# Optimization experiments

Hardware: AMD Instinct MI355X
Metric: run time of the kernel (lower is better)

The kernel has to match this reference:

```python
import jax, jax.numpy as jnp
import numpy as np

DIM, K_NN, RADIUS, HIDDEN = 128, 4, 2.5, 64
B, T, N = 32, 64, 25


def setup_inputs() -> dict:
    key = jax.random.key(0)
    ks = jax.random.split(key, 12)
    s = 0.02
    return {
        "emb": jax.random.normal(ks[0], (B, T, N, DIM), jnp.float32),
        "bboxes": jax.random.uniform(ks[1], (B, T, N, 4), jnp.float32),
        "person_mask": jax.random.uniform(ks[2], (B, T, N)) < 0.9,
        "edge_w1": jax.random.normal(ks[3], (2 * DIM + 3, HIDDEN), jnp.float32) * s,
        "edge_b1": jnp.zeros((HIDDEN,), jnp.float32),
        "edge_w2": jax.random.normal(ks[4], (HIDDEN, DIM), jnp.float32) * s,
        "edge_b2": jnp.zeros((DIM,), jnp.float32),
        "node_w1": jax.random.normal(ks[5], (2 * DIM, HIDDEN), jnp.float32) * s,
        "node_b1": jnp.zeros((HIDDEN,), jnp.float32),
        "node_w2": jax.random.normal(ks[6], (HIDDEN, DIM), jnp.float32) * s,
        "node_b2": jnp.zeros((DIM,), jnp.float32),
        "ln_g": jnp.ones((DIM,), jnp.float32),
        "ln_b": jnp.zeros((DIM,), jnp.float32),
    }


def _forward(emb, bboxes, person_mask, edge_w1, edge_b1, edge_w2, edge_b2,
             node_w1, node_b1, node_w2, node_b2, ln_g, ln_b):
    b, t, n, d = emb.shape
    BT = b * t
    x = emb.reshape(BT, n, d)
    boxes = bboxes.reshape(BT, n, 4)
    mask = person_mask.reshape(BT, n)

    cx, cy = boxes[..., 0], boxes[..., 1]
    h = jnp.maximum(boxes[..., 3], 1e-6)
    dx = cx[:, :, None] - cx[:, None, :]            # [BT,N,N]
    dy = cy[:, :, None] - cy[:, None, :]
    dist = jnp.sqrt(dx * dx + dy * dy + 1e-6)
    scale = h[:, :, None]
    dx_n, dy_n, dist_n = dx / scale, dy / scale, dist / scale

    eye = jnp.eye(n, dtype=bool)[None]
    pair_valid = (mask[:, :, None] & mask[:, None, :]) & ~eye
    dist_for_knn = jnp.where(pair_valid, dist_n, 1e6)

    K = min(K_NN, max(n - 1, 1))
    neg_d, knn_idx = jax.lax.top_k(-dist_for_knn, K)  # smallest-K -> [BT,N,K]
    knn_dist = -neg_d

    nbr_valid = jnp.take_along_axis(pair_valid, knn_idx, axis=2)
    nbr_valid = nbr_valid & (knn_dist < RADIUS)

    # gather neighbor features: [BT,N,K,D]
    bt_idx = jnp.arange(BT)[:, None, None]
    x_j = x[bt_idx, knn_idx]
    x_i = jnp.broadcast_to(x[:, :, None, :], (BT, n, K, d))
    edge_all = jnp.stack([dx_n, dy_n, dist_n], axis=-1)  # [BT,N,N,3]
    e_ij = jnp.take_along_axis(edge_all, knn_idx[..., None], axis=2)  # [BT,N,K,3]

    msg_in = jnp.concatenate([x_i, x_j, e_ij], axis=-1)  # [BT,N,K,2D+3]
    msg = jax.nn.relu(msg_in @ edge_w1 + edge_b1) @ edge_w2 + edge_b2
    nbr_f = nbr_valid.astype(msg.dtype)
    msg = msg * nbr_f[..., None]
    denom = jnp.maximum(nbr_f.sum(axis=2, keepdims=True), 1.0)
    agg = msg.sum(axis=2) / denom                    # [BT,N,D]

    upd_in = jnp.concatenate([x, agg], axis=-1)
    delta = jax.nn.relu(upd_in @ node_w1 + node_b1) @ node_w2 + node_b2
    has_nbr = jnp.any(nbr_valid, axis=2, keepdims=True)
    delta = delta * has_nbr.astype(delta.dtype)

    y = x + delta
    mu = y.mean(axis=-1, keepdims=True)
    var = y.var(axis=-1, keepdims=True)
    y = (y - mu) * jax.lax.rsqrt(var + 1e-5) * ln_g + ln_b
    out = y * mask[..., None].astype(y.dtype)
    return out.reshape(b, t, n, d)


def reference(emb, bboxes, person_mask, edge_w1, edge_b1, edge_w2, edge_b2,
              node_w1, node_b1, node_w2, node_b2, ln_g, ln_b):
    return _forward(emb, bboxes, person_mask, edge_w1, edge_b1, edge_w2, edge_b2,
                    node_w1, node_b1, node_w2, node_b2, ln_g, ln_b)
```

## Files before the change

kernel.cpp:

```cpp
#include <hip/hip_runtime.h>

#define NN   25
#define DD   128
#define HH   64
#define KK   4
#define RADF 2.5f

#define XBP  136
#define HSP  72
#define AGP  136

#define O_W1T 0
#define O_W2T 16896
#define O_N1T 25088
#define O_N2T 41472

typedef __attribute__((ext_vector_type(8))) short  short8;
typedef __attribute__((ext_vector_type(4))) float  f32x4;

__device__ __forceinline__ ushort f2bf(float x) {
    uint u = __float_as_uint(x);
    u += 0x7fffu + ((u >> 16) & 1u);
    return (ushort)(u >> 16);
}
__device__ __forceinline__ float bf2f(ushort u) {
    return __uint_as_float((uint)u << 16);
}
__device__ __forceinline__ uint pack2(float a, float b) {
    return (uint)f2bf(a) | ((uint)f2bf(b) << 16);
}
__device__ __forceinline__ short8 ldw(const ushort* p) {
    return *reinterpret_cast<const short8*>(p);
}
#define MFMA16(a, b, c) __builtin_amdgcn_mfma_f32_16x16x32_bf16((a), (b), (c), 0, 0, 0)

__global__ void prep_kernel(const float* __restrict__ ew1, const float* __restrict__ ew2,
                            const float* __restrict__ nw1, const float* __restrict__ nw2,
                            ushort* __restrict__ w) {
    int tid = blockIdx.x * blockDim.x + threadIdx.x;
    int stride = gridDim.x * blockDim.x;
    for (int e = tid; e < 259 * 64; e += stride) {
        int k = e >> 6, c = e & 63;
        w[O_W1T + c * 264 + k] = f2bf(ew1[e]);
    }
    for (int e = tid; e < 64 * 128; e += stride) {
        int k = e >> 7, d = e & 127;
        w[O_W2T + d * 64 + k] = f2bf(ew2[e]);
    }
    for (int e = tid; e < 256 * 64; e += stride) {
        int k = e >> 6, c = e & 63;
        w[O_N1T + c * 256 + k] = f2bf(nw1[e]);
    }
    for (int e = tid; e < 64 * 128; e += stride) {
        int k = e >> 7, d = e & 127;
        w[O_N2T + d * 64 + k] = f2bf(nw2[e]);
    }
}

__global__ __launch_bounds__(64, 2) void ig9_kernel(
    const float* __restrict__ emb,
    const float* __restrict__ bboxes,
    const int*   __restrict__ pmask,
    const float* __restrict__ ew1f,
    const float* __restrict__ eb1,
    const float* __restrict__ eb2,
    const float* __restrict__ nb1,
    const float* __restrict__ nb2,
    const float* __restrict__ lng,
    const float* __restrict__ lnb,
    const ushort* __restrict__ W,
    float* __restrict__ out)
{
    const int bt  = blockIdx.x;
    const int ln  = threadIdx.x;
    const int g   = ln >> 4;
    const int r16 = ln & 15;

    __shared__ ushort s_xb[NN * XBP];
    __shared__ __align__(16) char s_R[7200];
    __shared__ ushort s_g1v[NN * HSP];
    __shared__ float  s_ev[NN][KK][4];
    __shared__ short  s_idxs[NN][KK];
    __shared__ float  s_meta[NN][4];

    ushort* s_hxi = reinterpret_cast<ushort*>(s_R);
    ushort* s_hs  = reinterpret_cast<ushort*>(s_R + 3600);
    ushort* s_ag  = reinterpret_cast<ushort*>(s_R);

    {
        const float4* src4 = reinterpret_cast<const float4*>(emb + (size_t)bt * (NN * DD));
        for (int u = ln; u < NN * 16; u += 64) {
            int row = u >> 4, q = u & 15;
            float4 f0 = src4[row * 32 + q * 2];
            float4 f1 = src4[row * 32 + q * 2 + 1];
            uint4 p;
            p.x = pack2(f0.x, f0.y); p.y = pack2(f0.z, f0.w);
            p.z = pack2(f1.x, f1.y); p.w = pack2(f1.z, f1.w);
            *reinterpret_cast<uint4*>(&s_xb[row * XBP + q * 8]) = p;
        }
    }

    {
        const int n = (ln < NN) ? ln : NN - 1;
        const float4 b4 = *reinterpret_cast<const float4*>(bboxes + ((size_t)bt * NN + n) * 4);
        const float cxn = b4.x, cyn = b4.y;
        const float hvn = fmaxf(b4.w, 1e-6f);
        const int   mn  = pmask[(size_t)bt * NN + n];
        const float inv = 1.0f / hvn;
        float best[KK] = {1e30f, 1e30f, 1e30f, 1e30f};
        int   bidx[KK] = {0, 0, 0, 0};
        for (int j = 0; j < NN; ++j) {
            float cxj = __shfl(cxn, j);
            float cyj = __shfl(cyn, j);
            int   mj  = __shfl(mn, j);
            float dx = cxn - cxj, dy = cyn - cyj;
            float dn = sqrtf(fmaf(dx, dx, fmaf(dy, dy, 1e-6f))) * inv;
            bool  pv = (mn != 0) && (mj != 0) && (j != n);
            float cv = pv ? dn : 1e6f;
            int   ci = j;
#pragma unroll
            for (int kk = 0; kk < KK; ++kk) {
                if (cv < best[kk]) {
                    float tv = best[kk]; best[kk] = cv; cv = tv;
                    int   ti = bidx[kk]; bidx[kk] = ci; ci = ti;
                }
            }
        }
        float cnt = 0.f;
        float e0v[KK], e1v[KK], e2v[KK], vvv[KK];
#pragma unroll
        for (int k = 0; k < KK; ++k) {
            int bj = bidx[k];
            float cxb = __shfl(cxn, bj);
            float cyb = __shfl(cyn, bj);
            float val = (best[k] < RADF) ? 1.f : 0.f;
            cnt += val;
            float dx = cxn - cxb, dy = cyn - cyb;
            e0v[k] = dx * inv;
            e1v[k] = dy * inv;
            e2v[k] = sqrtf(fmaf(dx, dx, fmaf(dy, dy, 1e-6f))) * inv;
            vvv[k] = val;
        }
        if (ln < NN) {
#pragma unroll
            for (int k = 0; k < KK; ++k) {
                s_ev[n][k][0] = e0v[k];
                s_ev[n][k][1] = e1v[k];
                s_ev[n][k][2] = e2v[k];
                s_ev[n][k][3] = vvv[k];
                s_idxs[n][k]  = (short)bidx[k];
            }
            s_meta[n][0] = cnt;
            s_meta[n][1] = 1.0f / fmaxf(cnt, 1.0f);
            s_meta[n][2] = (cnt > 0.f) ? 1.f : 0.f;
            s_meta[n][3] = mn ? 1.f : 0.f;
        }
    }
    __syncthreads();

    {
        int na1 = 16 + r16; if (na1 > 24) na1 = 24;
        const ushort* A0 = s_xb + r16 * XBP + g * 8;
        const ushort* A1 = s_xb + na1 * XBP + g * 8;
        f32x4 c[2][4] = {};
#pragma unroll
        for (int kt = 0; kt < 4; ++kt) {
            short8 b[4];
#pragma unroll
            for (int nt = 0; nt < 4; ++nt)
                b[nt] = ldw(W + O_W1T + (size_t)(16 * nt + r16) * 264 + kt * 32 + g * 8);
            short8 a0 = ldw(A0 + kt * 32);
            short8 a1 = ldw(A1 + kt * 32);
#pragma unroll
            for (int nt = 0; nt < 4; ++nt) {
                c[0][nt] = MFMA16(a0, b[nt], c[0][nt]);
                c[1][nt] = MFMA16(a1, b[nt], c[1][nt]);
            }
        }
#pragma unroll
        for (int mt = 0; mt < 2; ++mt)
#pragma unroll
            for (int q = 0; q < 4; ++q) {
                int nr = 16 * mt + 4 * g + q;
                if (nr < 25) {
#pragma unroll
                    for (int nt = 0; nt < 4; ++nt)
                        s_hxi[nr * HSP + 16 * nt + r16] = f2bf(c[mt][nt][q]);
                }
            }
    }
    __syncthreads();

    {
        int jn[7];
#pragma unroll
        for (int T = 0; T < 7; ++T) {
            int r = 16 * T + r16; if (r > 99) r = 99;
            jn[T] = s_idxs[r >> 2][r & 3];
        }
        f32x4 c[7][4] = {};
#pragma unroll
        for (int kt = 0; kt < 4; ++kt) {
            short8 b[4];
#pragma unroll
            for (int nt = 0; nt < 4; ++nt)
                b[nt] = ldw(W + O_W1T + (size_t)(16 * nt + r16) * 264 + 128 + kt * 32 + g * 8);
#pragma unroll
            for (int T = 0; T < 7; ++T) {
                short8 a = ldw(s_xb + jn[T] * XBP + kt * 32 + g * 8);
#pragma unroll
                for (int nt = 0; nt < 4; ++nt)
                    c[T][nt] = MFMA16(a, b[nt], c[T][nt]);
            }
        }
        float we0[4], we1[4], we2[4], bb1[4];
#pragma unroll
        for (int nt = 0; nt < 4; ++nt) {
            int col = 16 * nt + r16;
            we0[nt] = ew1f[256 * 64 + col];
            we1[nt] = ew1f[257 * 64 + col];
            we2[nt] = ew1f[258 * 64 + col];
            bb1[nt] = eb1[col];
        }
#pragma unroll
        for (int T = 0; T < 7; ++T) {
            const int n = 4 * T + g;
            if (n < 25) {
                float v0 = s_ev[n][0][3], v1 = s_ev[n][1][3];
                float v2 = s_ev[n][2][3], v3 = s_ev[n][3][3];
                float e0q[4], e1q[4], e2q[4];
#pragma unroll
                for (int q = 0; q < 4; ++q) {
                    e0q[q] = s_ev[n][q][0]; e1q[q] = s_ev[n][q][1]; e2q[q] = s_ev[n][q][2];
                }
#pragma unroll
                for (int nt = 0; nt < 4; ++nt) {
                    int col = 16 * nt + r16;
                    float base = bb1[nt] + bf2f(s_hxi[n * HSP + col]);
                    float p0 = c[T][nt][0] + base + e0q[0] * we0[nt] + e1q[0] * we1[nt] + e2q[0] * we2[nt];
                    float p1 = c[T][nt][1] + base + e0q[1] * we0[nt] + e1q[1] * we1[nt] + e2q[1] * we2[nt];
                    float p2 = c[T][nt][2] + base + e0q[2] * we0[nt] + e1q[2] * we1[nt] + e2q[2] * we2[nt];
                    float p3 = c[T][nt][3] + base + e0q[3] * we0[nt] + e1q[3] * we1[nt] + e2q[3] * we2[nt];
                    float hs = fmaf(v0, fmaxf(p0, 0.f),
                               fmaf(v1, fmaxf(p1, 0.f),
                               fmaf(v2, fmaxf(p2, 0.f),
                                    v3 * fmaxf(p3, 0.f))));
                    s_hs[n * HSP + col] = f2bf(hs);
                }
            }
        }
    }
    __syncthreads();

    {
        int na1 = 16 + r16; if (na1 > 24) na1 = 24;
        const ushort* A0 = s_hs + r16 * HSP + g * 8;
        const ushort* A1 = s_hs + na1 * HSP + g * 8;
        f32x4 c[2][8] = {};
#pragma unroll
        for (int kt = 0; kt < 2; ++kt) {
            short8 a0 = ldw(A0 + kt * 32);
            short8 a1 = ldw(A1 + kt * 32);
#pragma unroll
            for (int nt = 0; nt < 8; ++nt) {
                short8 b = ldw(W + O_W2T + (size_t)(16 * nt + r16) * 64 + kt * 32 + g * 8);
                c[0][nt] = MFMA16(a0, b, c[0][nt]);
                c[1][nt] = MFMA16(a1, b, c[1][nt]);
            }
        }
        __syncthreads();
#pragma unroll
        for (int nt = 0; nt < 8; ++nt) {
            int col = 16 * nt + r16;
            float b2c = eb2[col];
#pragma unroll
            for (int mt = 0; mt < 2; ++mt)
#pragma unroll
                for (int q = 0; q < 4; ++q) {
                    int nr = 16 * mt + 4 * g + q;
                    if (nr < 25) {
                        float agv = s_meta[nr][1] * fmaf(s_meta[nr][0], b2c, c[mt][nt][q]);
                        s_ag[nr * AGP + col] = f2bf(agv);
                    }
                }
        }
    }
    __syncthreads();

    {
        int na1 = 16 + r16; if (na1 > 24) na1 = 24;
        const ushort* Ax0 = s_xb + r16 * XBP + g * 8;
        const ushort* Ax1 = s_xb + na1 * XBP + g * 8;
        const ushort* Aa0 = s_ag + r16 * AGP + g * 8;
        const ushort* Aa1 = s_ag + na1 * AGP + g * 8;
        f32x4 c[2][4] = {};
#pragma unroll
        for (int kt = 0; kt < 8; ++kt) {
            const ushort* Ap0 = (kt < 4) ? (Ax0 + kt * 32) : (Aa0 + (kt - 4) * 32);
            const ushort* Ap1 = (kt < 4) ? (Ax1 + kt * 32) : (Aa1 + (kt - 4) * 32);
            short8 a0 = ldw(Ap0);
            short8 a1 = ldw(Ap1);
#pragma unroll
            for (int nt = 0; nt < 4; ++nt) {
                short8 b = ldw(W + O_N1T + (size_t)(16 * nt + r16) * 256 + kt * 32 + g * 8);
                c[0][nt] = MFMA16(a0, b, c[0][nt]);
                c[1][nt] = MFMA16(a1, b, c[1][nt]);
            }
        }
#pragma unroll
        for (int nt = 0; nt < 4; ++nt) {
            int col = 16 * nt + r16;
            float b1c = nb1[col];
#pragma unroll
            for (int mt = 0; mt < 2; ++mt)
#pragma unroll
                for (int q = 0; q < 4; ++q) {
                    int nr = 16 * mt + 4 * g + q;
                    if (nr < 25)
                        s_g1v[nr * HSP + col] = f2bf(fmaxf(c[mt][nt][q] + b1c, 0.f));
                }
        }
    }
    __syncthreads();

    {
        int na1 = 16 + r16; if (na1 > 24) na1 = 24;
        const ushort* A0 = s_g1v + r16 * HSP + g * 8;
        const ushort* A1 = s_g1v + na1 * HSP + g * 8;
        f32x4 c[2][8] = {};
#pragma unroll
        for (int kt = 0; kt < 2; ++kt) {
            short8 a0 = ldw(A0 + kt * 32);
            short8 a1 = ldw(A1 + kt * 32);
#pragma unroll
            for (int nt = 0; nt < 8; ++nt) {
                short8 b = ldw(W + O_N2T + (size_t)(16 * nt + r16) * 64 + kt * 32 + g * 8);
                c[0][nt] = MFMA16(a0, b, c[0][nt]);
                c[1][nt] = MFMA16(a1, b, c[1][nt]);
            }
        }
        float nb2c[8], glc[8], blc[8];
#pragma unroll
        for (int nt = 0; nt < 8; ++nt) {
            int col = 16 * nt + r16;
            nb2c[nt] = nb2[col];
            glc[nt]  = lng[col];
            blc[nt]  = lnb[col];
        }
#pragma unroll
        for (int mt = 0; mt < 2; ++mt) {
#pragma unroll
            for (int q = 0; q < 4; ++q) {
                int nr = 16 * mt + 4 * g + q;
                int nc = nr < 25 ? nr : 24;
                float has = s_meta[nc][2];
                float y[8];
                float a = 0.f, b = 0.f;
#pragma unroll
                for (int nt = 0; nt < 8; ++nt) {
                    int col = 16 * nt + r16;
                    float yv = fmaf(has, c[mt][nt][q] + nb2c[nt], bf2f(s_xb[nc * XBP + col]));
                    y[nt] = yv;
                    a += yv;
                    b = fmaf(yv, yv, b);
                }
#pragma unroll
                for (int o = 1; o < 16; o <<= 1) {
                    a += __shfl_xor(a, o);
                    b += __shfl_xor(b, o);
                }
                float mu  = a * (1.0f / 128.0f);
                float var = b * (1.0f / 128.0f) - mu * mu;
                float rs  = rsqrtf(var + 1e-5f);
                float mk  = s_meta[nc][3];
                if (nr < 25) {
                    float* op = out + (size_t)bt * (NN * DD) + nr * DD;
#pragma unroll
                    for (int nt = 0; nt < 8; ++nt) {
                        int col = 16 * nt + r16;
                        op[col] = fmaf((y[nt] - mu) * rs, glc[nt], blc[nt]) * mk;
                    }
                }
            }
        }
    }
}

extern "C" void kernel_launch(void* const* d_in, const int* in_sizes, int n_in,
                              void* d_out, int out_size, void* d_ws, size_t ws_size,
                              hipStream_t stream) {
    const float* emb    = (const float*)d_in[0];
    const float* bboxes = (const float*)d_in[1];
    const int*   pmask  = (const int*)  d_in[2];
    const float* ew1    = (const float*)d_in[3];
    const float* eb1    = (const float*)d_in[4];
    const float* ew2    = (const float*)d_in[5];
    const float* eb2    = (const float*)d_in[6];
    const float* nw1    = (const float*)d_in[7];
    const float* nb1    = (const float*)d_in[8];
    const float* nw2    = (const float*)d_in[9];
    const float* nb2    = (const float*)d_in[10];
    const float* lng    = (const float*)d_in[11];
    const float* lnb    = (const float*)d_in[12];
    float* out = (float*)d_out;
    ushort* W  = (ushort*)d_ws;

    prep_kernel<<<64, 256, 0, stream>>>(ew1, ew2, nw1, nw2, W);

    const int BT = in_sizes[2] / NN;
    ig9_kernel<<<BT, 64, 0, stream>>>(
        emb, bboxes, pmask, ew1, eb1, eb2, nb1, nb2, lng, lnb, W, out);
}
```

Measured before the change: 48.53 us.

## Split fused GNN block across two waves by output column tiles

Launches 128 threads per block and splits each MFMA stage's output columns between two waves. Embedding load and kNN selection now run concurrently on separate waves. The LayerNorm reduction becomes a cross-wave reduction through shared memory. The goal is more parallelism per tile and fewer registers per wave, at the cost of an extra barrier and duplicated A-operand loads.

```diff
diff --git a/kernel.cpp b/kernel.cpp
--- a/kernel.cpp
+++ b/kernel.cpp
@@ -57,7 +57,7 @@
     }
 }
 
-__global__ __launch_bounds__(64, 2) void ig9_kernel(
+__global__ __launch_bounds__(128, 4) void ig10_kernel(
     const float* __restrict__ emb,
     const float* __restrict__ bboxes,
     const int*   __restrict__ pmask,
@@ -72,22 +72,28 @@
     float* __restrict__ out)
 {
     const int bt  = blockIdx.x;
-    const int ln  = threadIdx.x;
+    const int t   = threadIdx.x;
+    const int wv  = t >> 6;
+    const int ln  = t & 63;
     const int g   = ln >> 4;
     const int r16 = ln & 15;
+    const int cb  = 2 * wv;
+    const int cb4 = 4 * wv;
 
     __shared__ ushort s_xb[NN * XBP];
     __shared__ __align__(16) char s_R[7200];
     __shared__ ushort s_g1v[NN * HSP];
-    __shared__ float  s_ev[NN][KK][4];
+    __shared__ __align__(16) char s_misc[1600];
     __shared__ short  s_idxs[NN][KK];
     __shared__ float  s_meta[NN][4];
 
+    float (*s_ev)[KK][4] = reinterpret_cast<float(*)[KK][4]>(s_misc);
+    float (*s_red)[2][2] = reinterpret_cast<float(*)[2][2]>(s_misc);
     ushort* s_hxi = reinterpret_cast<ushort*>(s_R);
     ushort* s_hs  = reinterpret_cast<ushort*>(s_R + 3600);
     ushort* s_ag  = reinterpret_cast<ushort*>(s_R);
 
-    {
+    if (wv == 0) {
         const float4* src4 = reinterpret_cast<const float4*>(emb + (size_t)bt * (NN * DD));
         for (int u = ln; u < NN * 16; u += 64) {
             int row = u >> 4, q = u & 15;
@@ -98,9 +104,7 @@
             p.z = pack2(f1.x, f1.y); p.w = pack2(f1.z, f1.w);
             *reinterpret_cast<uint4*>(&s_xb[row * XBP + q * 8]) = p;
         }
-    }
-
-    {
+    } else {
         const int n = (ln < NN) ? ln : NN - 1;
         const float4 b4 = *reinterpret_cast<const float4*>(bboxes + ((size_t)bt * NN + n) * 4);
         const float cxn = b4.x, cyn = b4.y;
@@ -162,20 +166,15 @@
         int na1 = 16 + r16; if (na1 > 24) na1 = 24;
         const ushort* A0 = s_xb + r16 * XBP + g * 8;
         const ushort* A1 = s_xb + na1 * XBP + g * 8;
-        f32x4 c[2][4] = {};
+        f32x4 c[2][2] = {};
 #pragma unroll
         for (int kt = 0; kt < 4; ++kt) {
-            short8 b[4];
-#pragma unroll
-            for (int nt = 0; nt < 4; ++nt)
-                b[nt] = ldw(W + O_W1T + (size_t)(16 * nt + r16) * 264 + kt * 32 + g * 8);
+            short8 b0 = ldw(W + O_W1T + (size_t)(16 * (cb + 0) + r16) * 264 + kt * 32 + g * 8);
+            short8 b1 = ldw(W + O_W1T + (size_t)(16 * (cb + 1) + r16) * 264 + kt * 32 + g * 8);
             short8 a0 = ldw(A0 + kt * 32);
             short8 a1 = ldw(A1 + kt * 32);
-#pragma unroll
-            for (int nt = 0; nt < 4; ++nt) {
-                c[0][nt] = MFMA16(a0, b[nt], c[0][nt]);
-                c[1][nt] = MFMA16(a1, b[nt], c[1][nt]);
-            }
+            c[0][0] = MFMA16(a0, b0, c[0][0]); c[0][1] = MFMA16(a0, b1, c[0][1]);
+            c[1][0] = MFMA16(a1, b0, c[1][0]); c[1][1] = MFMA16(a1, b1, c[1][1]);
         }
 #pragma unroll
         for (int mt = 0; mt < 2; ++mt)
@@ -184,12 +183,11 @@
                 int nr = 16 * mt + 4 * g + q;
                 if (nr < 25) {
 #pragma unroll
-                    for (int nt = 0; nt < 4; ++nt)
-                        s_hxi[nr * HSP + 16 * nt + r16] = f2bf(c[mt][nt][q]);
-                }
-            }
-    }
-    __syncthreads();
+                    for (int ntl = 0; ntl < 2; ++ntl)
+                        s_hxi[nr * HSP + 16 * (cb + ntl) + r16] = f2bf(c[mt][ntl][q]);
+                }
+            }
+    }
 
     {
         int jn[7];
@@ -198,29 +196,26 @@
             int r = 16 * T + r16; if (r > 99) r = 99;
             jn[T] = s_idxs[r >> 2][r & 3];
         }
-        f32x4 c[7][4] = {};
+        f32x4 c[7][2] = {};
 #pragma unroll
         for (int kt = 0; kt < 4; ++kt) {
-            short8 b[4];
-#pragma unroll
-            for (int nt = 0; nt < 4; ++nt)
-                b[nt] = ldw(W + O_W1T + (size_t)(16 * nt + r16) * 264 + 128 + kt * 32 + g * 8);
+            short8 b0 = ldw(W + O_W1T + (size_t)(16 * (cb + 0) + r16) * 264 + 128 + kt * 32 + g * 8);
+            short8 b1 = ldw(W + O_W1T + (size_t)(16 * (cb + 1) + r16) * 264 + 128 + kt * 32 + g * 8);
 #pragma unroll
             for (int T = 0; T < 7; ++T) {
                 short8 a = ldw(s_xb + jn[T] * XBP + kt * 32 + g * 8);
-#pragma unroll
-                for (int nt = 0; nt < 4; ++nt)
-                    c[T][nt] = MFMA16(a, b[nt], c[T][nt]);
-            }
-        }
-        float we0[4], we1[4], we2[4], bb1[4];
-#pragma unroll
-        for (int nt = 0; nt < 4; ++nt) {
-            int col = 16 * nt + r16;
-            we0[nt] = ew1f[256 * 64 + col];
-            we1[nt] = ew1f[257 * 64 + col];
-            we2[nt] = ew1f[258 * 64 + col];
-            bb1[nt] = eb1[col];
+                c[T][0] = MFMA16(a, b0, c[T][0]);
+                c[T][1] = MFMA16(a, b1, c[T][1]);
+            }
+        }
+        float we0[2], we1[2], we2[2], bb1[2];
+#pragma unroll
+        for (int ntl = 0; ntl < 2; ++ntl) {
+            int col = 16 * (cb + ntl) + r16;
+            we0[ntl] = ew1f[256 * 64 + col];
+            we1[ntl] = ew1f[257 * 64 + col];
+            we2[ntl] = ew1f[258 * 64 + col];
+            bb1[ntl] = eb1[col];
         }
 #pragma unroll
         for (int T = 0; T < 7; ++T) {
@@ -234,13 +229,13 @@
                     e0q[q] = s_ev[n][q][0]; e1q[q] = s_ev[n][q][1]; e2q[q] = s_ev[n][q][2];
                 }
 #pragma unroll
-                for (int nt = 0; nt < 4; ++nt) {
-                    int col = 16 * nt + r16;
-                    float base = bb1[nt] + bf2f(s_hxi[n * HSP + col]);
-                    float p0 = c[T][nt][0] + base + e0q[0] * we0[nt] + e1q[0] * we1[nt] + e2q[0] * we2[nt];
-                    float p1 = c[T][nt][1] + base + e0q[1] * we0[nt] + e1q[1] * we1[nt] + e2q[1] * we2[nt];
-                    float p2 = c[T][nt][2] + base + e0q[2] * we0[nt] + e1q[2] * we1[nt] + e2q[2] * we2[nt];
-                    float p3 = c[T][nt][3] + base + e0q[3] * we0[nt] + e1q[3] * we1[nt] + e2q[3] * we2[nt];
+                for (int ntl = 0; ntl < 2; ++ntl) {
+                    int col = 16 * (cb + ntl) + r16;
+                    float base = bb1[ntl] + bf2f(s_hxi[n * HSP + col]);
+                    float p0 = c[T][ntl][0] + base + e0q[0] * we0[ntl] + e1q[0] * we1[ntl] + e2q[0] * we2[ntl];
+                    float p1 = c[T][ntl][1] + base + e0q[1] * we0[ntl] + e1q[1] * we1[ntl] + e2q[1] * we2[ntl];
+                    float p2 = c[T][ntl][2] + base + e0q[2] * we0[ntl] + e1q[2] * we1[ntl] + e2q[2] * we2[ntl];
+                    float p3 = c[T][ntl][3] + base + e0q[3] * we0[ntl] + e1q[3] * we1[ntl] + e2q[3] * we2[ntl];
                     float hs = fmaf(v0, fmaxf(p0, 0.f),
                                fmaf(v1, fmaxf(p1, 0.f),
                                fmaf(v2, fmaxf(p2, 0.f),
@@ -256,22 +251,22 @@
         int na1 = 16 + r16; if (na1 > 24) na1 = 24;
         const ushort* A0 = s_hs + r16 * HSP + g * 8;
         const ushort* A1 = s_hs + na1 * HSP + g * 8;
-        f32x4 c[2][8] = {};
+        f32x4 c[2][4] = {};
 #pragma unroll
         for (int kt = 0; kt < 2; ++kt) {
             short8 a0 = ldw(A0 + kt * 32);
             short8 a1 = ldw(A1 + kt * 32);
 #pragma unroll
-            for (int nt = 0; nt < 8; ++nt) {
-                short8 b = ldw(W + O_W2T + (size_t)(16 * nt + r16) * 64 + kt * 32 + g * 8);
-                c[0][nt] = MFMA16(a0, b, c[0][nt]);
-                c[1][nt] = MFMA16(a1, b, c[1][nt]);
+            for (int ntl = 0; ntl < 4; ++ntl) {
+                short8 b = ldw(W + O_W2T + (size_t)(16 * (cb4 + ntl) + r16) * 64 + kt * 32 + g * 8);
+                c[0][ntl] = MFMA16(a0, b, c[0][ntl]);
+                c[1][ntl] = MFMA16(a1, b, c[1][ntl]);
             }
         }
         __syncthreads();
 #pragma unroll
-        for (int nt = 0; nt < 8; ++nt) {
-            int col = 16 * nt + r16;
+        for (int ntl = 0; ntl < 4; ++ntl) {
+            int col = 16 * (cb4 + ntl) + r16;
             float b2c = eb2[col];
 #pragma unroll
             for (int mt = 0; mt < 2; ++mt)
@@ -279,7 +274,7 @@
                 for (int q = 0; q < 4; ++q) {
                     int nr = 16 * mt + 4 * g + q;
                     if (nr < 25) {
-                        float agv = s_meta[nr][1] * fmaf(s_meta[nr][0], b2c, c[mt][nt][q]);
+                        float agv = s_meta[nr][1] * fmaf(s_meta[nr][0], b2c, c[mt][ntl][q]);
                         s_ag[nr * AGP + col] = f2bf(agv);
                     }
                 }
@@ -293,7 +288,7 @@
         const ushort* Ax1 = s_xb + na1 * XBP + g * 8;
         const ushort* Aa0 = s_ag + r16 * AGP + g * 8;
         const ushort* Aa1 = s_ag + na1 * AGP + g * 8;
-        f32x4 c[2][4] = {};
+        f32x4 c[2][2] = {};
 #pragma unroll
         for (int kt = 0; kt < 8; ++kt) {
             const ushort* Ap0 = (kt < 4) ? (Ax0 + kt * 32) : (Aa0 + (kt - 4) * 32);
@@ -301,15 +296,15 @@
             short8 a0 = ldw(Ap0);
             short8 a1 = ldw(Ap1);
 #pragma unroll
-            for (int nt = 0; nt < 4; ++nt) {
-                short8 b = ldw(W + O_N1T + (size_t)(16 * nt + r16) * 256 + kt * 32 + g * 8);
-                c[0][nt] = MFMA16(a0, b, c[0][nt]);
-                c[1][nt] = MFMA16(a1, b, c[1][nt]);
-            }
-        }
-#pragma unroll
-        for (int nt = 0; nt < 4; ++nt) {
-            int col = 16 * nt + r16;
+            for (int ntl = 0; ntl < 2; ++ntl) {
+                short8 b = ldw(W + O_N1T + (size_t)(16 * (cb + ntl) + r16) * 256 + kt * 32 + g * 8);
+                c[0][ntl] = MFMA16(a0, b, c[0][ntl]);
+                c[1][ntl] = MFMA16(a1, b, c[1][ntl]);
+            }
+        }
+#pragma unroll
+        for (int ntl = 0; ntl < 2; ++ntl) {
+            int col = 16 * (cb + ntl) + r16;
             float b1c = nb1[col];
 #pragma unroll
             for (int mt = 0; mt < 2; ++mt)
@@ -317,7 +312,7 @@
                 for (int q = 0; q < 4; ++q) {
                     int nr = 16 * mt + 4 * g + q;
                     if (nr < 25)
-                        s_g1v[nr * HSP + col] = f2bf(fmaxf(c[mt][nt][q] + b1c, 0.f));
+                        s_g1v[nr * HSP + col] = f2bf(fmaxf(c[mt][ntl][q] + b1c, 0.f));
                 }
         }
     }
@@ -327,26 +322,27 @@
         int na1 = 16 + r16; if (na1 > 24) na1 = 24;
         const ushort* A0 = s_g1v + r16 * HSP + g * 8;
         const ushort* A1 = s_g1v + na1 * HSP + g * 8;
-        f32x4 c[2][8] = {};
+        f32x4 c[2][4] = {};
 #pragma unroll
         for (int kt = 0; kt < 2; ++kt) {
             short8 a0 = ldw(A0 + kt * 32);
             short8 a1 = ldw(A1 + kt * 32);
 #pragma unroll
-            for (int nt = 0; nt < 8; ++nt) {
-                short8 b = ldw(W + O_N2T + (size_t)(16 * nt + r16) * 64 + kt * 32 + g * 8);
-                c[0][nt] = MFMA16(a0, b, c[0][nt]);
-                c[1][nt] = MFMA16(a1, b, c[1][nt]);
-            }
-        }
-        float nb2c[8], glc[8], blc[8];
-#pragma unroll
-        for (int nt = 0; nt < 8; ++nt) {
-            int col = 16 * nt + r16;
-            nb2c[nt] = nb2[col];
-            glc[nt]  = lng[col];
-            blc[nt]  = lnb[col];
-        }
+            for (int ntl = 0; ntl < 4; ++ntl) {
+                short8 b = ldw(W + O_N2T + (size_t)(16 * (cb4 + ntl) + r16) * 64 + kt * 32 + g * 8);
+                c[0][ntl] = MFMA16(a0, b, c[0][ntl]);
+                c[1][ntl] = MFMA16(a1, b, c[1][ntl]);
+            }
+        }
+        float nb2c[4], glc[4], blc[4];
+#pragma unroll
+        for (int ntl = 0; ntl < 4; ++ntl) {
+            int col = 16 * (cb4 + ntl) + r16;
+            nb2c[ntl] = nb2[col];
+            glc[ntl]  = lng[col];
+            blc[ntl]  = lnb[col];
+        }
+        float y[2][4][4];
 #pragma unroll
         for (int mt = 0; mt < 2; ++mt) {
 #pragma unroll
@@ -354,13 +350,12 @@
                 int nr = 16 * mt + 4 * g + q;
                 int nc = nr < 25 ? nr : 24;
                 float has = s_meta[nc][2];
-                float y[8];
                 float a = 0.f, b = 0.f;
 #pragma unroll
-                for (int nt = 0; nt < 8; ++nt) {
-                    int col = 16 * nt + r16;
-                    float yv = fmaf(has, c[mt][nt][q] + nb2c[nt], bf2f(s_xb[nc * XBP + col]));
-                    y[nt] = yv;
+                for (int ntl = 0; ntl < 4; ++ntl) {
+                    int col = 16 * (cb4 + ntl) + r16;
+                    float yv = fmaf(has, c[mt][ntl][q] + nb2c[ntl], bf2f(s_xb[nc * XBP + col]));
+                    y[mt][ntl][q] = yv;
                     a += yv;
                     b = fmaf(yv, yv, b);
                 }
@@ -369,16 +364,31 @@
                     a += __shfl_xor(a, o);
                     b += __shfl_xor(b, o);
                 }
-                float mu  = a * (1.0f / 128.0f);
-                float var = b * (1.0f / 128.0f) - mu * mu;
+                if (r16 == 0 && nr < 25) {
+                    s_red[nr][wv][0] = a;
+                    s_red[nr][wv][1] = b;
+                }
+            }
+        }
+        __syncthreads();
+#pragma unroll
+        for (int mt = 0; mt < 2; ++mt) {
+#pragma unroll
+            for (int q = 0; q < 4; ++q) {
+                int nr = 16 * mt + 4 * g + q;
+                int nc = nr < 25 ? nr : 24;
+                float S   = s_red[nc][0][0] + s_red[nc][1][0];
+                float S2  = s_red[nc][0][1] + s_red[nc][1][1];
+                float mu  = S * (1.0f / 128.0f);
+                float var = S2 * (1.0f / 128.0f) - mu * mu;
                 float rs  = rsqrtf(var + 1e-5f);
                 float mk  = s_meta[nc][3];
                 if (nr < 25) {
                     float* op = out + (size_t)bt * (NN * DD) + nr * DD;
 #pragma unroll
-                    for (int nt = 0; nt < 8; ++nt) {
-                        int col = 16 * nt + r16;
-                        op[col] = fmaf((y[nt] - mu) * rs, glc[nt], blc[nt]) * mk;
+                    for (int ntl = 0; ntl < 4; ++ntl) {
+                        int col = 16 * (cb4 + ntl) + r16;
+                        op[col] = fmaf((y[mt][ntl][q] - mu) * rs, glc[ntl], blc[ntl]) * mk;
                     }
                 }
             }
@@ -408,6 +418,6 @@
     prep_kernel<<<64, 256, 0, stream>>>(ew1, ew2, nw1, nw2, W);
 
     const int BT = in_sizes[2] / NN;
-    ig9_kernel<<<BT, 64, 0, stream>>>(
+    ig10_kernel<<<BT, 128, 0, stream>>>(
         emb, bboxes, pmask, ew1, eb1, eb2, nb1, nb2, lng, lnb, W, out);
 }
```

Result: faster. 42.63 us (-12.2%).
